# Optimization experiments

Measured on AMD Instinct MI355X. Metric: run time of the kernel, lower is better.

## Reference

```python
import jax, jax.numpy as jnp
import numpy as np

SAMPLING_RATE = 0.5

def setup_inputs() -> dict:
    key = jax.random.key(0)
    k1, k2 = jax.random.split(key)
    token = jax.random.normal(k1, (8, 16, 4, 384), dtype=jnp.float32)
    feature = jax.random.normal(k2, (8, 16, 4, 196, 384), dtype=jnp.float32)
    return {"token": token, "feature": feature}

def reference(token, feature):
    b1, n1, kk1, c = token.shape
    b2, n2, kk2, hw, _ = feature.shape
    N = n1 * kk1  # == n2 * kk2
    tok = token.reshape(b1, N, 1, c)           # [b, N, 1, c]
    feat = feature.reshape(b2, N, hw, c)       # [b, N, hw, c]
    scale = c ** (-0.5)
    # attention scores: [b, N, 1, hw]
    attn = jnp.einsum('bnqc,bnhc->bnqh', tok, feat) * scale
    attn = jax.nn.softmax(attn, axis=-1)
    tk = int(hw * SAMPLING_RATE)
    sel_attn, sel_idx = jax.lax.top_k(attn, tk)          # [b, N, 1, tk]
    sel_attn = sel_attn / jnp.sum(sel_attn, axis=-1, keepdims=True)
    # gather selected features: idx [b, N, tk] -> feat rows [b, N, tk, c]
    idx = sel_idx[:, :, 0, :]                            # [b, N, tk]
    sel_feat = jnp.take_along_axis(feat, idx[..., None], axis=2)  # [b, N, tk, c]
    out = jnp.einsum('bnqt,bntc->bnqc', sel_attn, sel_feat)       # [b, N, 1, c]
    return out.reshape(b1, n1, kk1, c)
```

## Files before the change

kernel.cpp:

```cpp
#include <hip/hip_runtime.h>

#define HW 196
#define C  384
#define CF4 (C/4)
#define TK 98
#define NT 512
#define NWAVE (NT/64)

__global__ __launch_bounds__(NT, 4) void sampling_kernel(
    const float* __restrict__ token,
    const float* __restrict__ feature,
    float* __restrict__ out)
{
    __shared__ float tokLds[C];
    __shared__ float score[HW];
    __shared__ float selW[TK];
    __shared__ int   selIdx[TK];
    __shared__ float wsum[NWAVE];
    __shared__ int   rank2[2 * HW];
    __shared__ float part[NWAVE][C];
    __shared__ float s_max, s_winv;

    const int tid  = threadIdx.x;
    const int wave = tid >> 6;
    const int lane = tid & 63;
    const int g    = lane >> 2;
    const int l    = lane & 3;
    const int pair = blockIdx.x;

    const float* tokp  = token   + (size_t)pair * C;
    const float* featp = feature + (size_t)pair * (HW * C);
    const float4* f4base = (const float4*)featp;
    const float4* t4     = (const float4*)tokLds;

    for (int i = tid; i < C; i += NT) tokLds[i] = tokp[i];
    __syncthreads();

    const float scale = 0.05103103630798288f;

    {
        const int r0 = wave * 16 + g;
        const float4* f0 = f4base + (size_t)r0 * CF4 + l;
        float4 a[12], b[12];
        #pragma unroll
        for (int k = 0; k < 12; ++k) a[k] = f0[4 * k];
        #pragma unroll
        for (int k = 0; k < 12; ++k) b[k] = f0[4 * (k + 12)];
        __builtin_amdgcn_sched_barrier(0);
        float4 acc = make_float4(0.f, 0.f, 0.f, 0.f);
        #pragma unroll
        for (int k = 0; k < 12; ++k) {
            float4 t = t4[l + 4 * k];
            acc.x += a[k].x * t.x; acc.y += a[k].y * t.y;
            acc.z += a[k].z * t.z; acc.w += a[k].w * t.w;
        }
        #pragma unroll
        for (int k = 0; k < 12; ++k) {
            float4 t = t4[l + 4 * (k + 12)];
            acc.x += b[k].x * t.x; acc.y += b[k].y * t.y;
            acc.z += b[k].z * t.z; acc.w += b[k].w * t.w;
        }
        float s = (acc.x + acc.y) + (acc.z + acc.w);
        s += __shfl_xor(s, 1, 64);
        s += __shfl_xor(s, 2, 64);
        if (l == 0) score[r0] = s * scale;

        if (r0 < HW - 128) {
            const int r1 = 128 + r0;
            const float4* f1 = f4base + (size_t)r1 * CF4 + l;
            #pragma unroll
            for (int k = 0; k < 12; ++k) a[k] = f1[4 * k];
            #pragma unroll
            for (int k = 0; k < 12; ++k) b[k] = f1[4 * (k + 12)];
            __builtin_amdgcn_sched_barrier(0);
            float4 acc1 = make_float4(0.f, 0.f, 0.f, 0.f);
            #pragma unroll
            for (int k = 0; k < 12; ++k) {
                float4 t = t4[l + 4 * k];
                acc1.x += a[k].x * t.x; acc1.y += a[k].y * t.y;
                acc1.z += a[k].z * t.z; acc1.w += a[k].w * t.w;
            }
            #pragma unroll
            for (int k = 0; k < 12; ++k) {
                float4 t = t4[l + 4 * (k + 12)];
                acc1.x += b[k].x * t.x; acc1.y += b[k].y * t.y;
                acc1.z += b[k].z * t.z; acc1.w += b[k].w * t.w;
            }
            float s1 = (acc1.x + acc1.y) + (acc1.z + acc1.w);
            s1 += __shfl_xor(s1, 1, 64);
            s1 += __shfl_xor(s1, 2, 64);
            if (l == 0) score[r1] = s1 * scale;
        }
    }
    __syncthreads();

    if (tid < 2 * HW) {
        const int i = tid >> 1, h = tid & 1;
        const float si = score[i];
        int cnt = 0;
        const int j0 = h * (HW / 2);
        for (int j = j0; j < j0 + HW / 2; ++j) {
            const float sj = score[j];
            cnt += (int)((sj > si) | ((sj == si) & (j < i)));
        }
        rank2[tid] = cnt;
    } else if (wave == NWAVE - 1) {
        float m = -3.4e38f;
        for (int i = lane; i < HW; i += 64) m = fmaxf(m, score[i]);
        #pragma unroll
        for (int off = 32; off > 0; off >>= 1)
            m = fmaxf(m, __shfl_xor(m, off, 64));
        if (lane == 0) s_max = m;
    }
    __syncthreads();

    float w = 0.f;
    if (tid < HW) {
        const int rank = rank2[2 * tid] + rank2[2 * tid + 1];
        if (rank < TK) {
            w = __expf(score[tid] - s_max);
            selIdx[rank] = tid;
            selW[rank]  = w;
        }
    }
    #pragma unroll
    for (int off = 32; off > 0; off >>= 1) w += __shfl_xor(w, off, 64);
    if (lane == 0) wsum[wave] = w;
    __syncthreads();
    if (tid == 0) {
        float s = 0.f;
        #pragma unroll
        for (int i = 0; i < NWAVE; ++i) s += wsum[i];
        s_winv = 1.f / s;
    }
    __syncthreads();

    float4 acc_a = make_float4(0.f, 0.f, 0.f, 0.f);
    float4 acc_b = make_float4(0.f, 0.f, 0.f, 0.f);
    #pragma unroll
    for (int j = 0; j < 12; ++j) {
        const int i = wave + NWAVE * j;
        const int   r   = selIdx[i];
        const float wgt = selW[i];
        const float4* f4 = f4base + (size_t)r * CF4;
        float4 aa = f4[lane];
        acc_a.x += wgt * aa.x; acc_a.y += wgt * aa.y;
        acc_a.z += wgt * aa.z; acc_a.w += wgt * aa.w;
        if (lane < 32) {
            float4 bb = f4[64 + lane];
            acc_b.x += wgt * bb.x; acc_b.y += wgt * bb.y;
            acc_b.z += wgt * bb.z; acc_b.w += wgt * bb.w;
        }
    }
    if (wave < TK - 96) {
        const int i = 96 + wave;
        const int   r   = selIdx[i];
        const float wgt = selW[i];
        const float4* f4 = f4base + (size_t)r * CF4;
        float4 aa = f4[lane];
        acc_a.x += wgt * aa.x; acc_a.y += wgt * aa.y;
        acc_a.z += wgt * aa.z; acc_a.w += wgt * aa.w;
        if (lane < 32) {
            float4 bb = f4[64 + lane];
            acc_b.x += wgt * bb.x; acc_b.y += wgt * bb.y;
            acc_b.z += wgt * bb.z; acc_b.w += wgt * bb.w;
        }
    }
    float4* pw = (float4*)&part[wave][0];
    pw[lane] = acc_a;
    if (lane < 32) pw[64 + lane] = acc_b;
    __syncthreads();

    if (tid < C) {
        float s = 0.f;
        #pragma unroll
        for (int wv = 0; wv < NWAVE; ++wv) s += part[wv][tid];
        out[(size_t)pair * C + tid] = s * s_winv;
    }
}

extern "C" void kernel_launch(void* const* d_in, const int* in_sizes, int n_in,
                              void* d_out, int out_size, void* d_ws, size_t ws_size,
                              hipStream_t stream) {
    const float* token   = (const float*)d_in[0];
    const float* feature = (const float*)d_in[1];
    float* out = (float*)d_out;
    const int pairs = in_sizes[0] / C;
    sampling_kernel<<<pairs, NT, 0, stream>>>(token, feature, out);
}
```

Baseline: 38.50 us.

## Use 8 lanes per score row and cache token in registers

The score phase now assigns 8 lanes per feature row instead of 4, covering 196 rows in three 64-row passes plus a small tail handled by the first four waves. The token slice each lane needs is loaded from LDS into registers once and reused across all passes, removing the repeated LDS reads. Each lane loads 12 float4 per row instead of 24, which lowers register pressure but adds loop iterations and a third shuffle step. The tail branch runs with only 8 active lanes per wave, which wastes some lanes.

Result: no change. 38.11 us (-1.0%).

```diff
diff --git a/kernel.cpp b/kernel.cpp
--- a/kernel.cpp
+++ b/kernel.cpp
@@ -24,8 +24,8 @@
     const int tid  = threadIdx.x;
     const int wave = tid >> 6;
     const int lane = tid & 63;
-    const int g    = lane >> 2;
-    const int l    = lane & 3;
+    const int l8   = lane & 7;
+    const int g8   = lane >> 3;
     const int pair = blockIdx.x;
 
     const float* tokp  = token   + (size_t)pair * C;
@@ -36,61 +36,46 @@
     for (int i = tid; i < C; i += NT) tokLds[i] = tokp[i];
     __syncthreads();
 
+    float4 tok[12];
+    #pragma unroll
+    for (int k = 0; k < 12; ++k) tok[k] = t4[l8 + 8 * k];
+
     const float scale = 0.05103103630798288f;
 
-    {
-        const int r0 = wave * 16 + g;
-        const float4* f0 = f4base + (size_t)r0 * CF4 + l;
-        float4 a[12], b[12];
+    #pragma unroll
+    for (int it = 0; it < 3; ++it) {
+        const int r = it * 64 + wave * 8 + g8;
+        const float4* fr = f4base + (size_t)r * CF4 + l8;
+        float4 a[12];
         #pragma unroll
-        for (int k = 0; k < 12; ++k) a[k] = f0[4 * k];
-        #pragma unroll
-        for (int k = 0; k < 12; ++k) b[k] = f0[4 * (k + 12)];
-        __builtin_amdgcn_sched_barrier(0);
+        for (int k = 0; k < 12; ++k) a[k] = fr[8 * k];
         float4 acc = make_float4(0.f, 0.f, 0.f, 0.f);
         #pragma unroll
         for (int k = 0; k < 12; ++k) {
-            float4 t = t4[l + 4 * k];
-            acc.x += a[k].x * t.x; acc.y += a[k].y * t.y;
-            acc.z += a[k].z * t.z; acc.w += a[k].w * t.w;
-        }
-        #pragma unroll
-        for (int k = 0; k < 12; ++k) {
-            float4 t = t4[l + 4 * (k + 12)];
-            acc.x += b[k].x * t.x; acc.y += b[k].y * t.y;
-            acc.z += b[k].z * t.z; acc.w += b[k].w * t.w;
+            acc.x += a[k].x * tok[k].x; acc.y += a[k].y * tok[k].y;
+            acc.z += a[k].z * tok[k].z; acc.w += a[k].w * tok[k].w;
         }
         float s = (acc.x + acc.y) + (acc.z + acc.w);
         s += __shfl_xor(s, 1, 64);
         s += __shfl_xor(s, 2, 64);
-        if (l == 0) score[r0] = s * scale;
-
-        if (r0 < HW - 128) {
-            const int r1 = 128 + r0;
-            const float4* f1 = f4base + (size_t)r1 * CF4 + l;
-            #pragma unroll
-            for (int k = 0; k < 12; ++k) a[k] = f1[4 * k];
-            #pragma unroll
-            for (int k = 0; k < 12; ++k) b[k] = f1[4 * (k + 12)];
-            __builtin_amdgcn_sched_barrier(0);
-            float4 acc1 = make_float4(0.f, 0.f, 0.f, 0.f);
-            #pragma unroll
-            for (int k = 0; k < 12; ++k) {
-                float4 t = t4[l + 4 * k];
-                acc1.x += a[k].x * t.x; acc1.y += a[k].y * t.y;
-                acc1.z += a[k].z * t.z; acc1.w += a[k].w * t.w;
-            }
-            #pragma unroll
-            for (int k = 0; k < 12; ++k) {
-                float4 t = t4[l + 4 * (k + 12)];
-                acc1.x += b[k].x * t.x; acc1.y += b[k].y * t.y;
-                acc1.z += b[k].z * t.z; acc1.w += b[k].w * t.w;
-            }
-            float s1 = (acc1.x + acc1.y) + (acc1.z + acc1.w);
-            s1 += __shfl_xor(s1, 1, 64);
-            s1 += __shfl_xor(s1, 2, 64);
-            if (l == 0) score[r1] = s1 * scale;
+        s += __shfl_xor(s, 4, 64);
+        if (l8 == 0) score[r] = s * scale;
+    }
+    if (wave < 4 && g8 == 0) {
+        const int r = 192 + wave;
+        const float4* fr = f4base + (size_t)r * CF4 + l8;
+        float4 acc = make_float4(0.f, 0.f, 0.f, 0.f);
+        #pragma unroll
+        for (int k = 0; k < 12; ++k) {
+            float4 a = fr[8 * k];
+            acc.x += a.x * tok[k].x; acc.y += a.y * tok[k].y;
+            acc.z += a.z * tok[k].z; acc.w += a.w * tok[k].w;
         }
+        float s = (acc.x + acc.y) + (acc.z + acc.w);
+        s += __shfl_xor(s, 1, 64);
+        s += __shfl_xor(s, 2, 64);
+        s += __shfl_xor(s, 4, 64);
+        if (l8 == 0) score[r] = s * scale;
     }
     __syncthreads();
 
```
